# Performance work log

Hardware: AMD Instinct MI355X
Metric: run time of the kernel (lower is better)

Reference implementation:

```python
import jax, jax.numpy as jnp
import numpy as np

N_NODES = 200000
N_EDGES = 3200000
N_FEAT = 128
N_GRAPHS = 1000
N_CLASSES = 10
K = 30          # sort-pool k
C_CAT = 97      # 32+32+32+1 concatenated channels


def _glorot(k, shape):
    fan = shape[0] + shape[-1]
    return jax.random.normal(k, shape, jnp.float32) * (2.0 / fan) ** 0.5


def setup_inputs() -> dict:
    key = jax.random.key(0)
    ks = jax.random.split(key, 20)
    x = jax.random.normal(ks[0], (N_NODES, N_FEAT), jnp.float32)
    edge_index = jax.random.randint(ks[1], (2, N_EDGES), 0, N_NODES, jnp.int32)
    batch = jnp.sort(jax.random.randint(ks[2], (N_NODES,), 0, N_GRAPHS, jnp.int32))
    params = dict(
        W1=_glorot(ks[3], (N_FEAT, 32)), b1=jnp.zeros((32,), jnp.float32),
        W2=_glorot(ks[4], (32, 32)),     b2=jnp.zeros((32,), jnp.float32),
        W3=_glorot(ks[5], (32, 32)),     b3=jnp.zeros((32,), jnp.float32),
        W4=_glorot(ks[6], (32, 1)),      b4=jnp.zeros((1,), jnp.float32),
        conv5_w=_glorot(ks[7], (16, 1, 97)),  conv5_b=jnp.zeros((16,), jnp.float32),
        conv6_w=_glorot(ks[8], (32, 16, 5)),  conv6_b=jnp.zeros((32,), jnp.float32),
        fc1_w=_glorot(ks[9], (352, 128)),     fc1_b=jnp.zeros((128,), jnp.float32),
        fc2_w=_glorot(ks[10], (128, N_CLASSES)), fc2_b=jnp.zeros((N_CLASSES,), jnp.float32),
    )
    return dict(x=x, edge_index=edge_index, batch=batch, **params)


def reference(x, edge_index, batch, W1, b1, W2, b2, W3, b3, W4, b4,
              conv5_w, conv5_b, conv6_w, conv6_b, fc1_w, fc1_b, fc2_w, fc2_b):
    N = x.shape[0]
    src, dst = edge_index[0], edge_index[1]
    emask = (src != dst).astype(x.dtype)            # remove_self_loops
    deg = jax.ops.segment_sum(emask, dst, num_segments=N) + 1.0  # +1 for added self-loop
    inv_sqrt = jax.lax.rsqrt(deg)
    coef = emask * inv_sqrt[src] * inv_sqrt[dst]    # D^-1/2 (A) D^-1/2 edge weight
    inv_deg = 1.0 / deg                             # self-loop weight

    def gcn(h, W, b):
        hw = h @ W
        agg = jax.ops.segment_sum(hw[src] * coef[:, None], dst, num_segments=N)
        return agg + hw * inv_deg[:, None] + b

    x1 = jnp.tanh(gcn(x, W1, b1))
    x2 = jnp.tanh(gcn(x1, W2, b2))
    x3 = jnp.tanh(gcn(x2, W3, b3))
    x4 = jnp.tanh(gcn(x3, W4, b4))
    xc = jnp.concatenate([x1, x2, x3, x4], axis=-1)  # [N, 97]

    # SortAggregation(k=30): per-graph descending sort by last channel, top-k, zero pad
    perm = jnp.lexsort((-xc[:, -1], batch))          # batch-major, last channel desc
    xs, bs = xc[perm], batch[perm]
    counts = jax.ops.segment_sum(jnp.ones_like(batch), batch, num_segments=N_GRAPHS)
    starts = jnp.cumsum(counts) - counts
    rank = jnp.arange(N, dtype=jnp.int32) - starts[bs]
    valid = rank < K
    pooled = jnp.zeros((N_GRAPHS, K, C_CAT), xc.dtype).at[
        bs, jnp.where(valid, rank, K - 1)].add(jnp.where(valid[:, None], xs, 0.0))

    z = pooled.reshape(N_GRAPHS, 1, K * C_CAT)       # [G, 1, 2910]
    dn = ('NCH', 'OIH', 'NCH')
    z = jax.lax.conv_general_dilated(z, conv5_w, (97,), 'VALID', dimension_numbers=dn)
    z = jax.nn.relu(z + conv5_b[None, :, None])      # [G, 16, 30]
    z = jax.lax.reduce_window(z, -jnp.inf, jax.lax.max, (1, 1, 2), (1, 1, 2), 'VALID')
    z = jax.lax.conv_general_dilated(z, conv6_w, (1,), 'VALID', dimension_numbers=dn)
    z = jax.nn.relu(z + conv6_b[None, :, None])      # [G, 32, 11]
    z = z.reshape(N_GRAPHS, -1)                      # [G, 352]
    h = jax.nn.relu(z @ fc1_w + fc1_b)               # dropout is identity in eval
    return jax.nn.log_softmax(h @ fc2_w + fc2_b, axis=-1)
```

## Files before the change

### kernel.cpp

```cpp
#include <hip/hip_runtime.h>
#include <math.h>

#define NN 200000
#define NE 3200000
#define NF 128
#define NG 1000
#define KSEL 30
#define CCAT 97
#define NPAD 200704
#define SCAN_BLKS 196

#define BWID 512
#define NB 391
#define BCAP 10240
#define P1_CHUNK 8192
#define P1_BLKS 391

__global__ void k_p1_partition(const int* __restrict__ ei, int* __restrict__ bcursor,
                               int* __restrict__ ebuf) {
    __shared__ int lhist[NB];
    __shared__ int lbase[NB];
    int tid = threadIdx.x;
    int base = blockIdx.x * P1_CHUNK;
    for (int b = tid; b < NB; b += 256) lhist[b] = 0;
    __syncthreads();
    for (int it = 0; it < P1_CHUNK / 256; it++) {
        int e = base + it * 256 + tid;
        if (e < NE) {
            int s = ei[e], d = ei[NE + e];
            if (s != d) atomicAdd(&lhist[d >> 9], 1);
        }
    }
    __syncthreads();
    for (int b = tid; b < NB; b += 256) {
        int cnt = lhist[b];
        lbase[b] = cnt ? atomicAdd(&bcursor[b], cnt) : 0;
        lhist[b] = 0;
    }
    __syncthreads();
    for (int it = 0; it < P1_CHUNK / 256; it++) {
        int e = base + it * 256 + tid;
        if (e < NE) {
            int s = ei[e], d = ei[NE + e];
            if (s != d) {
                int b = d >> 9;
                int r = atomicAdd(&lhist[b], 1);
                int pos = lbase[b] + r;
                if (pos >= BCAP) pos = BCAP - 1;
                ebuf[b * BCAP + pos] = s | ((d & 511) << 18);
            }
        }
    }
}

__global__ void k_p2_count(const int* __restrict__ bcursor, const int* __restrict__ ebuf,
                           int* __restrict__ rowcnt, float* __restrict__ inv_sqrt) {
    __shared__ int lcnt[BWID];
    int b = blockIdx.x;
    int tid = threadIdx.x;
    for (int i = tid; i < BWID; i += 256) lcnt[i] = 0;
    __syncthreads();
    int size = bcursor[b];
    if (size > BCAP) size = BCAP;
    const int* eb = ebuf + b * BCAP;
    for (int k = tid; k < size; k += 256) atomicAdd(&lcnt[eb[k] >> 18], 1);
    __syncthreads();
    int node0 = b * BWID;
    for (int i = tid; i < BWID; i += 256) {
        int node = node0 + i;
        if (node < NN) {
            int c = lcnt[i];
            rowcnt[node] = c;
            inv_sqrt[node] = rsqrtf((float)(c + 1));
        }
    }
}

__global__ void k_scanA(const int* __restrict__ in, int* __restrict__ out,
                        int* __restrict__ bsums) {
    __shared__ int s[1024];
    int tid = threadIdx.x;
    int gid = blockIdx.x * 1024 + tid;
    int v = in[gid];
    s[tid] = v;
    __syncthreads();
    for (int off = 1; off < 1024; off <<= 1) {
        int a = (tid >= off) ? s[tid - off] : 0;
        int cur = s[tid];
        __syncthreads();
        s[tid] = cur + a;
        __syncthreads();
    }
    out[gid] = s[tid] - v;
    if (tid == 1023) bsums[blockIdx.x] = s[tid];
}

__global__ void k_scanB(int* __restrict__ bsums) {
    __shared__ int s[256];
    int tid = threadIdx.x;
    int v = (tid < SCAN_BLKS) ? bsums[tid] : 0;
    s[tid] = v;
    __syncthreads();
    for (int off = 1; off < 256; off <<= 1) {
        int a = (tid >= off) ? s[tid - off] : 0;
        int cur = s[tid];
        __syncthreads();
        s[tid] = cur + a;
        __syncthreads();
    }
    if (tid < SCAN_BLKS) bsums[tid] = s[tid] - v;
}

__global__ void k_scanC(int* __restrict__ out, const int* __restrict__ bsums) {
    int gid = blockIdx.x * 1024 + threadIdx.x;
    out[gid] += bsums[blockIdx.x];
}

__global__ void k_p3_scatter(const int* __restrict__ bcursor, const int* __restrict__ ebuf,
                             const int* __restrict__ rowstart, int* __restrict__ esrc) {
    __shared__ int lcur[BWID];
    int b = blockIdx.x;
    int tid = threadIdx.x;
    int node0 = b * BWID;
    for (int i = tid; i < BWID; i += 256) lcur[i] = rowstart[node0 + i];
    __syncthreads();
    int size = bcursor[b];
    if (size > BCAP) size = BCAP;
    const int* eb = ebuf + b * BCAP;
    for (int k = tid; k < size; k += 256) {
        int v = eb[k];
        int local = v >> 18;
        int pos = atomicAdd(&lcur[local], 1);
        esrc[pos] = v & 0x3FFFF;
    }
}

template <int K>
__global__ void __launch_bounds__(128, 5) k_mm(const float* __restrict__ X,
                                               const float* __restrict__ W,
                                               const float* __restrict__ inv_sqrt,
                                               float* __restrict__ Y) {
    __shared__ float4 sW[K * 8];
    int tid = threadIdx.x;
    for (int i = tid; i < K * 8; i += 128) sW[i] = ((const float4*)W)[i];
    __syncthreads();
    int g = tid >> 3;
    int q = tid & 7;
    int r0 = blockIdx.x * 64 + g * 4;
    if (r0 >= NN) return;
    const float4* __restrict__ xp0 = (const float4*)(X + (size_t)(r0 + 0) * K);
    const float4* __restrict__ xp1 = (const float4*)(X + (size_t)(r0 + 1) * K);
    const float4* __restrict__ xp2 = (const float4*)(X + (size_t)(r0 + 2) * K);
    const float4* __restrict__ xp3 = (const float4*)(X + (size_t)(r0 + 3) * K);
    float4 a0 = make_float4(0.f, 0.f, 0.f, 0.f);
    float4 a1 = make_float4(0.f, 0.f, 0.f, 0.f);
    float4 a2 = make_float4(0.f, 0.f, 0.f, 0.f);
    float4 a3 = make_float4(0.f, 0.f, 0.f, 0.f);
#pragma unroll 2
    for (int k4 = 0; k4 < K / 4; k4++) {
        float4 x0 = xp0[k4];
        float4 x1 = xp1[k4];
        float4 x2 = xp2[k4];
        float4 x3 = xp3[k4];
        const float4* wk = &sW[k4 * 32 + q];
#pragma unroll
        for (int kk = 0; kk < 4; kk++) {
            float4 w = wk[kk * 8];
            float s0 = (kk == 0) ? x0.x : (kk == 1) ? x0.y : (kk == 2) ? x0.z : x0.w;
            float s1 = (kk == 0) ? x1.x : (kk == 1) ? x1.y : (kk == 2) ? x1.z : x1.w;
            float s2 = (kk == 0) ? x2.x : (kk == 1) ? x2.y : (kk == 2) ? x2.z : x2.w;
            float s3 = (kk == 0) ? x3.x : (kk == 1) ? x3.y : (kk == 2) ? x3.z : x3.w;
            a0.x = fmaf(s0, w.x, a0.x); a0.y = fmaf(s0, w.y, a0.y);
            a0.z = fmaf(s0, w.z, a0.z); a0.w = fmaf(s0, w.w, a0.w);
            a1.x = fmaf(s1, w.x, a1.x); a1.y = fmaf(s1, w.y, a1.y);
            a1.z = fmaf(s1, w.z, a1.z); a1.w = fmaf(s1, w.w, a1.w);
            a2.x = fmaf(s2, w.x, a2.x); a2.y = fmaf(s2, w.y, a2.y);
            a2.z = fmaf(s2, w.z, a2.z); a2.w = fmaf(s2, w.w, a2.w);
            a3.x = fmaf(s3, w.x, a3.x); a3.y = fmaf(s3, w.y, a3.y);
            a3.z = fmaf(s3, w.z, a3.z); a3.w = fmaf(s3, w.w, a3.w);
        }
    }
    float s0 = inv_sqrt[r0 + 0];
    float s1 = inv_sqrt[r0 + 1];
    float s2 = inv_sqrt[r0 + 2];
    float s3 = inv_sqrt[r0 + 3];
    a0.x *= s0; a0.y *= s0; a0.z *= s0; a0.w *= s0;
    a1.x *= s1; a1.y *= s1; a1.z *= s1; a1.w *= s1;
    a2.x *= s2; a2.y *= s2; a2.z *= s2; a2.w *= s2;
    a3.x *= s3; a3.y *= s3; a3.z *= s3; a3.w *= s3;
    ((float4*)(Y + (size_t)(r0 + 0) * 32))[q] = a0;
    ((float4*)(Y + (size_t)(r0 + 1) * 32))[q] = a1;
    ((float4*)(Y + (size_t)(r0 + 2) * 32))[q] = a2;
    ((float4*)(Y + (size_t)(r0 + 3) * 32))[q] = a3;
}

__global__ void k_aggr(const int* __restrict__ rowstart, const int* __restrict__ esrc,
                       const float* __restrict__ hws, const float* __restrict__ inv_sqrt,
                       const float* __restrict__ b, float* __restrict__ xout) {
    int t = blockIdx.x * 256 + threadIdx.x;
    int n = t >> 5, c = t & 31;
    if (n >= NN) return;
    int e0 = rowstart[n], e1 = rowstart[n + 1];
    float a[8];
    a[0] = hws[(size_t)n * 32 + c];
#pragma unroll
    for (int k = 1; k < 8; k++) a[k] = 0.0f;
    for (int e = e0; e < e1; e += 8) {
        int ss[8];
#pragma unroll
        for (int k = 0; k < 8; k++) ss[k] = esrc[(e + k < e1) ? e + k : e];
        float vv[8];
#pragma unroll
        for (int k = 0; k < 8; k++) vv[k] = hws[(size_t)ss[k] * 32 + c];
        a[0] += vv[0];
#pragma unroll
        for (int k = 1; k < 8; k++) a[k] += (e + k < e1) ? vv[k] : 0.0f;
    }
    float acc = ((a[0] + a[1]) + (a[2] + a[3])) + ((a[4] + a[5]) + (a[6] + a[7]));
    xout[t] = tanhf(fmaf(acc, inv_sqrt[n], b[c]));
}

__global__ void k_mm4(const float* __restrict__ x3, const float* __restrict__ W4,
                      const float* __restrict__ inv_sqrt, float* __restrict__ hws4) {
    int n = blockIdx.x * 256 + threadIdx.x;
    if (n >= NN) return;
    const float4* xr = (const float4*)(x3 + (size_t)n * 32);
    float acc = 0.0f;
#pragma unroll
    for (int q = 0; q < 8; q++) {
        float4 v = xr[q];
        acc = fmaf(v.x, W4[q * 4 + 0], acc);
        acc = fmaf(v.y, W4[q * 4 + 1], acc);
        acc = fmaf(v.z, W4[q * 4 + 2], acc);
        acc = fmaf(v.w, W4[q * 4 + 3], acc);
    }
    hws4[n] = acc * inv_sqrt[n];
}

__global__ void k_aggr1(const int* __restrict__ rowstart, const int* __restrict__ esrc,
                        const float* __restrict__ hws4, const float* __restrict__ inv_sqrt,
                        const float* __restrict__ b4, float* __restrict__ x4) {
    int n = blockIdx.x * 256 + threadIdx.x;
    if (n >= NN) return;
    int e0 = rowstart[n], e1 = rowstart[n + 1];
    float a[8];
    a[0] = hws4[n];
#pragma unroll
    for (int k = 1; k < 8; k++) a[k] = 0.0f;
    for (int e = e0; e < e1; e += 8) {
        int ss[8];
#pragma unroll
        for (int k = 0; k < 8; k++) ss[k] = esrc[(e + k < e1) ? e + k : e];
        float vv[8];
#pragma unroll
        for (int k = 0; k < 8; k++) vv[k] = hws4[ss[k]];
        a[0] += vv[0];
#pragma unroll
        for (int k = 1; k < 8; k++) a[k] += (e + k < e1) ? vv[k] : 0.0f;
    }
    float acc = ((a[0] + a[1]) + (a[2] + a[3])) + ((a[4] + a[5]) + (a[6] + a[7]));
    x4[n] = tanhf(fmaf(acc, inv_sqrt[n], b4[0]));
}

__global__ void k_gbounds(const int* __restrict__ batch, int* __restrict__ starts) {
    int n = blockIdx.x * 256 + threadIdx.x;
    if (n >= NN) return;
    int bn = batch[n];
    int bp = (n == 0) ? -1 : batch[n - 1];
    for (int g = bp + 1; g <= bn; g++) starts[g] = n;
    if (n == NN - 1)
        for (int g = bn + 1; g <= NG; g++) starts[g] = NN;
}

__global__ void k_sortpool(const int* __restrict__ starts,
                           const float* __restrict__ x1, const float* __restrict__ x2,
                           const float* __restrict__ x3, const float* __restrict__ x4,
                           float* __restrict__ pooled) {
    __shared__ float keys[1024];
    __shared__ int sel[KSEL];
    int g = blockIdx.x;
    int tid = threadIdx.x;
    int start = starts[g];
    int cnt = starts[g + 1] - start;
    if (cnt > 1024) cnt = 1024;
    for (int i = tid; i < cnt; i += 256) keys[i] = x4[start + i];
    __syncthreads();
    for (int i = tid; i < cnt; i += 256) {
        float ki = keys[i];
        int rank = 0;
        for (int j = 0; j < cnt; j++) {
            float kj = keys[j];
            rank += (kj > ki) || (kj == ki && j < i);
        }
        if (rank < KSEL) sel[rank] = start + i;
    }
    __syncthreads();
    int selcnt = cnt < KSEL ? cnt : KSEL;
    for (int t = tid; t < KSEL * CCAT; t += 256) {
        int r = t / CCAT, ch = t - r * CCAT;
        float v = 0.0f;
        if (r < selcnt) {
            int node = sel[r];
            if (ch < 32)      v = x1[(size_t)node * 32 + ch];
            else if (ch < 64) v = x2[(size_t)node * 32 + ch - 32];
            else if (ch < 96) v = x3[(size_t)node * 32 + ch - 64];
            else              v = x4[node];
        }
        pooled[g * (KSEL * CCAT) + t] = v;
    }
}

__global__ void k_head(const float* __restrict__ pooled,
                       const float* __restrict__ w5, const float* __restrict__ b5,
                       const float* __restrict__ w6, const float* __restrict__ b6,
                       const float* __restrict__ fw1, const float* __restrict__ fb1,
                       const float* __restrict__ fw2, const float* __restrict__ fb2,
                       float* __restrict__ out) {
    __shared__ float sP[KSEL * CCAT];
    __shared__ float s5[16 * 30];
    __shared__ float smp[16 * 15];
    __shared__ float sz[352];
    __shared__ float sh[128];
    __shared__ float sl[10];
    int g = blockIdx.x;
    int tid = threadIdx.x;
    for (int i = tid; i < KSEL * CCAT; i += 256) sP[i] = pooled[g * (KSEL * CCAT) + i];
    __syncthreads();
    for (int t = tid; t < 16 * 30; t += 256) {
        int c = t / 30, j = t - c * 30;
        float acc = b5[c];
        for (int i = 0; i < CCAT; i++) acc = fmaf(sP[j * CCAT + i], w5[c * CCAT + i], acc);
        s5[c * 30 + j] = fmaxf(acc, 0.0f);
    }
    __syncthreads();
    for (int t = tid; t < 16 * 15; t += 256) {
        int c = t / 15, j = t - c * 15;
        smp[t] = fmaxf(s5[c * 30 + 2 * j], s5[c * 30 + 2 * j + 1]);
    }
    __syncthreads();
    for (int t = tid; t < 32 * 11; t += 256) {
        int c = t / 11, j = t - c * 11;
        float acc = b6[c];
        for (int ci = 0; ci < 16; ci++) {
#pragma unroll
            for (int k = 0; k < 5; k++)
                acc = fmaf(smp[ci * 15 + j + k], w6[(c * 16 + ci) * 5 + k], acc);
        }
        sz[t] = fmaxf(acc, 0.0f);
    }
    __syncthreads();
    if (tid < 128) {
        float acc = fb1[tid];
        for (int i = 0; i < 352; i++) acc = fmaf(sz[i], fw1[i * 128 + tid], acc);
        sh[tid] = fmaxf(acc, 0.0f);
    }
    __syncthreads();
    if (tid < 10) {
        float acc = fb2[tid];
        for (int i = 0; i < 128; i++) acc = fmaf(sh[i], fw2[i * 10 + tid], acc);
        sl[tid] = acc;
    }
    __syncthreads();
    if (tid < 10) {
        float m = -1e30f;
        for (int i = 0; i < 10; i++) m = fmaxf(m, sl[i]);
        float ssum = 0.0f;
        for (int i = 0; i < 10; i++) ssum += expf(sl[i] - m);
        out[g * 10 + tid] = sl[tid] - m - logf(ssum);
    }
}

extern "C" void kernel_launch(void* const* d_in, const int* in_sizes, int n_in,
                              void* d_out, int out_size, void* d_ws, size_t ws_size,
                              hipStream_t stream) {
    const float* x   = (const float*)d_in[0];
    const int*   ei  = (const int*)d_in[1];
    const int*   bat = (const int*)d_in[2];
    const float* W1  = (const float*)d_in[3];
    const float* b1  = (const float*)d_in[4];
    const float* W2  = (const float*)d_in[5];
    const float* b2  = (const float*)d_in[6];
    const float* W3  = (const float*)d_in[7];
    const float* b3  = (const float*)d_in[8];
    const float* W4  = (const float*)d_in[9];
    const float* b4  = (const float*)d_in[10];
    const float* w5  = (const float*)d_in[11];
    const float* b5  = (const float*)d_in[12];
    const float* w6  = (const float*)d_in[13];
    const float* b6  = (const float*)d_in[14];
    const float* fw1 = (const float*)d_in[15];
    const float* fb1 = (const float*)d_in[16];
    const float* fw2 = (const float*)d_in[17];
    const float* fb2 = (const float*)d_in[18];
    float* out = (float*)d_out;

    float* ws = (float*)d_ws;
    float* inv_sqrt = ws;
    float* hws      = inv_sqrt + NN;
    float* x1       = hws + (size_t)NN * 32;
    float* x2       = x1 + (size_t)NN * 32;
    float* x3       = x2 + (size_t)NN * 32;
    float* x4       = x3 + (size_t)NN * 32;
    float* pooled   = x4 + NN;
    int* rowcnt     = (int*)(pooled + NG * KSEL * CCAT);
    int* rowstart   = rowcnt + NPAD;
    int* esrc       = rowstart + NPAD;
    int* bcursor    = esrc + NE;
    int* bsums      = bcursor + 512;
    int* gstarts    = bsums + 256;
    int* ebuf       = (int*)x3;

    const int TB = 256;
    int gN  = (NN + TB - 1) / TB;
    int gNC = (NN * 32 + TB - 1) / TB;
    int gMM = (NN + 63) / 64;

    hipMemsetAsync(bcursor, 0, 512 * sizeof(int), stream);
    hipMemsetAsync(rowcnt, 0, NPAD * sizeof(int), stream);
    k_p1_partition<<<P1_BLKS, TB, 0, stream>>>(ei, bcursor, ebuf);
    k_p2_count<<<NB, TB, 0, stream>>>(bcursor, ebuf, rowcnt, inv_sqrt);
    k_scanA<<<SCAN_BLKS, 1024, 0, stream>>>(rowcnt, rowstart, bsums);
    k_scanB<<<1, 256, 0, stream>>>(bsums);
    k_scanC<<<SCAN_BLKS, 1024, 0, stream>>>(rowstart, bsums);
    k_p3_scatter<<<NB, TB, 0, stream>>>(bcursor, ebuf, rowstart, esrc);

    k_gbounds<<<gN, TB, 0, stream>>>(bat, gstarts);

    k_mm<128><<<gMM, 128, 0, stream>>>(x, W1, inv_sqrt, hws);
    k_aggr<<<gNC, TB, 0, stream>>>(rowstart, esrc, hws, inv_sqrt, b1, x1);
    k_mm<32><<<gMM, 128, 0, stream>>>(x1, W2, inv_sqrt, hws);
    k_aggr<<<gNC, TB, 0, stream>>>(rowstart, esrc, hws, inv_sqrt, b2, x2);
    k_mm<32><<<gMM, 128, 0, stream>>>(x2, W3, inv_sqrt, hws);
    k_aggr<<<gNC, TB, 0, stream>>>(rowstart, esrc, hws, inv_sqrt, b3, x3);
    k_mm4<<<gN, TB, 0, stream>>>(x3, W4, inv_sqrt, hws);
    k_aggr1<<<gN, TB, 0, stream>>>(rowstart, esrc, hws, inv_sqrt, b4, x4);

    k_sortpool<<<NG, TB, 0, stream>>>(gstarts, x1, x2, x3, x4, pooled);
    k_head<<<NG, TB, 0, stream>>>(pooled, w5, b5, w6, b6, fw1, fb1, fw2, fb2, out);
}
```

Baseline: 601.4 us.

## Pad CSR rows to multiples of eight with dummy zero node for vector index loads

Rounds each node's neighbour count up to a multiple of eight and fills the padding slots with a sentinel index pointing to an extra zero row appended to the feature buffers. The aggregation kernels can then load source indices as two aligned int4 vectors and drop the per-edge bounds checks and selects. In exchange the edge array grows, some gathers now hit the dummy row, and the scatter kernel gets an extra padding-fill loop. It also relies on the hws4 buffer having room for the sentinel entry.

```diff
diff --git a/kernel.cpp b/kernel.cpp
--- a/kernel.cpp
+++ b/kernel.cpp
@@ -9,6 +9,7 @@
 #define CCAT 97
 #define NPAD 200704
 #define SCAN_BLKS 196
+#define EPADCAP (NE + 8 * NN)
 
 #define BWID 512
 #define NB 391
@@ -70,7 +71,7 @@
         int node = node0 + i;
         if (node < NN) {
             int c = lcnt[i];
-            rowcnt[node] = c;
+            rowcnt[node] = (c + 7) & ~7;
             inv_sqrt[node] = rsqrtf((float)(c + 1));
         }
     }
@@ -132,6 +133,14 @@
         int local = v >> 18;
         int pos = atomicAdd(&lcur[local], 1);
         esrc[pos] = v & 0x3FFFF;
+    }
+    __syncthreads();
+    for (int i = tid; i < BWID; i += 256) {
+        int node = node0 + i;
+        if (node < NN) {
+            int end = rowstart[node + 1];
+            for (int p = lcur[i]; p < end; p++) esrc[p] = NN;
+        }
     }
 }
 
@@ -206,15 +215,18 @@
 #pragma unroll
     for (int k = 1; k < 8; k++) a[k] = 0.0f;
     for (int e = e0; e < e1; e += 8) {
-        int ss[8];
-#pragma unroll
-        for (int k = 0; k < 8; k++) ss[k] = esrc[(e + k < e1) ? e + k : e];
-        float vv[8];
-#pragma unroll
-        for (int k = 0; k < 8; k++) vv[k] = hws[(size_t)ss[k] * 32 + c];
-        a[0] += vv[0];
-#pragma unroll
-        for (int k = 1; k < 8; k++) a[k] += (e + k < e1) ? vv[k] : 0.0f;
+        int4 sA = *(const int4*)(esrc + e);
+        int4 sB = *(const int4*)(esrc + e + 4);
+        float v0 = hws[(size_t)sA.x * 32 + c];
+        float v1 = hws[(size_t)sA.y * 32 + c];
+        float v2 = hws[(size_t)sA.z * 32 + c];
+        float v3 = hws[(size_t)sA.w * 32 + c];
+        float v4 = hws[(size_t)sB.x * 32 + c];
+        float v5 = hws[(size_t)sB.y * 32 + c];
+        float v6 = hws[(size_t)sB.z * 32 + c];
+        float v7 = hws[(size_t)sB.w * 32 + c];
+        a[0] += v0; a[1] += v1; a[2] += v2; a[3] += v3;
+        a[4] += v4; a[5] += v5; a[6] += v6; a[7] += v7;
     }
     float acc = ((a[0] + a[1]) + (a[2] + a[3])) + ((a[4] + a[5]) + (a[6] + a[7]));
     xout[t] = tanhf(fmaf(acc, inv_sqrt[n], b[c]));
@@ -224,6 +236,7 @@
                       const float* __restrict__ inv_sqrt, float* __restrict__ hws4) {
     int n = blockIdx.x * 256 + threadIdx.x;
     if (n >= NN) return;
+    if (n == 0) hws4[NN] = 0.0f;
     const float4* xr = (const float4*)(x3 + (size_t)n * 32);
     float acc = 0.0f;
 #pragma unroll
@@ -248,15 +261,12 @@
 #pragma unroll
     for (int k = 1; k < 8; k++) a[k] = 0.0f;
     for (int e = e0; e < e1; e += 8) {
-        int ss[8];
-#pragma unroll
-        for (int k = 0; k < 8; k++) ss[k] = esrc[(e + k < e1) ? e + k : e];
-        float vv[8];
-#pragma unroll
-        for (int k = 0; k < 8; k++) vv[k] = hws4[ss[k]];
-        a[0] += vv[0];
-#pragma unroll
-        for (int k = 1; k < 8; k++) a[k] += (e + k < e1) ? vv[k] : 0.0f;
+        int4 sA = *(const int4*)(esrc + e);
+        int4 sB = *(const int4*)(esrc + e + 4);
+        a[0] += hws4[sA.x]; a[1] += hws4[sA.y];
+        a[2] += hws4[sA.z]; a[3] += hws4[sA.w];
+        a[4] += hws4[sB.x]; a[5] += hws4[sB.y];
+        a[6] += hws4[sB.z]; a[7] += hws4[sB.w];
     }
     float acc = ((a[0] + a[1]) + (a[2] + a[3])) + ((a[4] + a[5]) + (a[6] + a[7]));
     x4[n] = tanhf(fmaf(acc, inv_sqrt[n], b4[0]));
@@ -397,7 +407,7 @@
     float* ws = (float*)d_ws;
     float* inv_sqrt = ws;
     float* hws      = inv_sqrt + NN;
-    float* x1       = hws + (size_t)NN * 32;
+    float* x1       = hws + (size_t)(NN + 1) * 32;
     float* x2       = x1 + (size_t)NN * 32;
     float* x3       = x2 + (size_t)NN * 32;
     float* x4       = x3 + (size_t)NN * 32;
@@ -405,7 +415,7 @@
     int* rowcnt     = (int*)(pooled + NG * KSEL * CCAT);
     int* rowstart   = rowcnt + NPAD;
     int* esrc       = rowstart + NPAD;
-    int* bcursor    = esrc + NE;
+    int* bcursor    = esrc + EPADCAP;
     int* bsums      = bcursor + 512;
     int* gstarts    = bsums + 256;
     int* ebuf       = (int*)x3;
@@ -417,6 +427,7 @@
 
     hipMemsetAsync(bcursor, 0, 512 * sizeof(int), stream);
     hipMemsetAsync(rowcnt, 0, NPAD * sizeof(int), stream);
+    hipMemsetAsync(hws + (size_t)NN * 32, 0, 32 * sizeof(float), stream);
     k_p1_partition<<<P1_BLKS, TB, 0, stream>>>(ei, bcursor, ebuf);
     k_p2_count<<<NB, TB, 0, stream>>>(bcursor, ebuf, rowcnt, inv_sqrt);
     k_scanA<<<SCAN_BLKS, 1024, 0, stream>>>(rowcnt, rowstart, bsums);
```

Result: no change. 599.8 us (-0.3%).
